# Optimization experiments

Hardware: AMD Instinct MI355X
Metric: run time of the kernel (lower is better)

Reference implementation:

```python
import jax, jax.numpy as jnp
import numpy as np

SEQ_LEN, BATCH, D_IN, D_H, D_OUT = 512, 64, 1024, 1024, 1024
W_SCALE = 0.02  # small init so sigmoid/tanh stay in a sane range


def setup_inputs() -> dict:
    key = jax.random.key(0)
    ks = jax.random.split(key, 12)
    rn = lambda k, shape: jax.random.normal(k, shape, dtype=jnp.float32)
    return {
        "x_seq": rn(ks[0], (SEQ_LEN, BATCH, D_IN)),
        "h0": jnp.zeros((BATCH, D_H), dtype=jnp.float32),
        "Wxz_w": rn(ks[1], (D_H, D_IN)) * W_SCALE,
        "Wxz_b": rn(ks[2], (D_H,)) * W_SCALE,
        "Whz_w": rn(ks[3], (D_H, D_H)) * W_SCALE,
        "Wxr_w": rn(ks[4], (D_H, D_IN)) * W_SCALE,
        "Wxr_b": rn(ks[5], (D_H,)) * W_SCALE,
        "Whr_w": rn(ks[6], (D_H, D_H)) * W_SCALE,
        "Wxn_w": rn(ks[7], (D_H, D_IN)) * W_SCALE,
        "Wxn_b": rn(ks[8], (D_H,)) * W_SCALE,
        "Whn_w": rn(ks[9], (D_H, D_H)) * W_SCALE,
        "Why_w": rn(ks[10], (D_OUT, D_H)) * W_SCALE,
        "Why_b": rn(ks[11], (D_OUT,)) * W_SCALE,
    }


def reference(x_seq, h0, Wxz_w, Wxz_b, Whz_w, Wxr_w, Wxr_b, Whr_w,
              Wxn_w, Wxn_b, Whn_w, Why_w, Why_b):
    # Precompute all input projections in one batched GEMM per gate:
    # (S, B, D_in) @ (D_in, D_h) -> (S, B, D_h). torch Linear: x @ W.T + b.
    xz = jnp.einsum('sbi,hi->sbh', x_seq, Wxz_w) + Wxz_b
    xr = jnp.einsum('sbi,hi->sbh', x_seq, Wxr_w) + Wxr_b
    xn = jnp.einsum('sbi,hi->sbh', x_seq, Wxn_w) + Wxn_b

    def step(h, xs):
        xz_t, xr_t, xn_t = xs
        z = jax.nn.sigmoid(xz_t + h @ Whz_w.T)
        r = jax.nn.sigmoid(xr_t + h @ Whr_w.T)
        n = jnp.tanh(xn_t + (r * h) @ Whn_w.T)
        h_new = (1.0 - z) * h + z * n
        return h_new, h_new

    h_last, hs = jax.lax.scan(step, h0, (xz, xr, xn))  # hs: (S, B, D_h)
    outputs = jnp.einsum('sbh,oh->sbo', hs, Why_w) + Why_b
    return outputs, h_last
```

## Files before the change

### kernel.cpp

```cpp
#include <hip/hip_runtime.h>

typedef unsigned int uint;
typedef unsigned short ushort;
typedef unsigned long long u64;

typedef short s8v __attribute__((ext_vector_type(8)));
typedef float f4v __attribute__((ext_vector_type(4)));

#define S_LEN 512
#define BATCH 64
#define DH    1024
#define DIN   1024

union B8 { s8v v; uint u[4]; u64 ull[2]; ushort s[8]; };

__device__ inline ushort f2bf(float f){
  uint u = __builtin_bit_cast(uint, f);
  u += 0x7fffu + ((u >> 16) & 1u);
  return (ushort)(u >> 16);
}
__device__ inline float bf2f(ushort s){
  uint u = ((uint)s) << 16;
  return __builtin_bit_cast(float, u);
}

__device__ inline f4v mfma16(s8v a, s8v b, f4v c){
  return __builtin_amdgcn_mfma_f32_16x16x32_bf16(a, b, c, 0, 0, 0);
}

__device__ inline s8v ld_b8(const ushort* p){
  return *reinterpret_cast<const s8v*>(p);
}

__device__ inline s8v ld_b8_llc(const ushort* p){
  B8 b;
  const u64* q = (const u64*)p;
  b.ull[0] = __hip_atomic_load(q,   __ATOMIC_RELAXED, __HIP_MEMORY_SCOPE_AGENT);
  b.ull[1] = __hip_atomic_load(q+1, __ATOMIC_RELAXED, __HIP_MEMORY_SCOPE_AGENT);
  return b.v;
}

__device__ inline uint ald32(const uint* p){
  return __hip_atomic_load(p, __ATOMIC_RELAXED, __HIP_MEMORY_SCOPE_AGENT);
}
__device__ inline void ast32(uint* p, uint v){
  __hip_atomic_store(p, v, __ATOMIC_RELAXED, __HIP_MEMORY_SCOPE_AGENT);
}

__device__ inline s8v cvt8(float4 a, float4 b){
  B8 r;
  r.s[0]=f2bf(a.x); r.s[1]=f2bf(a.y); r.s[2]=f2bf(a.z); r.s[3]=f2bf(a.w);
  r.s[4]=f2bf(b.x); r.s[5]=f2bf(b.y); r.s[6]=f2bf(b.z); r.s[7]=f2bf(b.w);
  return r.v;
}

__global__ void cvt_kernel(const float* __restrict__ src, ushort* __restrict__ dst, int n){
  int i = (blockIdx.x * blockDim.x + threadIdx.x) * 4;
  if (i + 3 < n){
    float4 v = *reinterpret_cast<const float4*>(src + i);
    u64 p = (u64)f2bf(v.x)
          | ((u64)f2bf(v.y) << 16)
          | ((u64)f2bf(v.z) << 32)
          | ((u64)f2bf(v.w) << 48);
    *reinterpret_cast<u64*>(dst + i) = p;
  }
}

__global__ void __launch_bounds__(256, 1)
proj3_kernel(const float* __restrict__ X,
             const ushort* __restrict__ W0, const ushort* __restrict__ W1, const ushort* __restrict__ W2,
             const float* __restrict__ bias0, const float* __restrict__ bias1, const float* __restrict__ bias2,
             ushort* __restrict__ C0, ushort* __restrict__ C1, ushort* __restrict__ C2)
{
  const int lane = threadIdx.x & 63;
  const int wave = threadIdx.x >> 6;
  const int l15  = lane & 15;
  const int krow = (lane >> 4) << 3;
  const int n0 = blockIdx.x * 64;
  const int m0 = blockIdx.y * 128 + wave * 32;

  const ushort* Ws[3] = {W0, W1, W2};
  const float*  Bs[3] = {bias0, bias1, bias2};
  ushort*       Cs[3] = {C0, C1, C2};

  f4v acc[2][3][4];
  #pragma unroll
  for (int ms = 0; ms < 2; ++ms)
    #pragma unroll
    for (int g = 0; g < 3; ++g)
      #pragma unroll
      for (int nn = 0; nn < 4; ++nn)
        acc[ms][g][nn] = (f4v){0.f,0.f,0.f,0.f};

  const float* a0 = X + (m0 + l15) * DIN + krow;
  const float* a1 = a0 + 16 * DIN;

  for (int k = 0; k < DIN; k += 32){
    s8v af[2];
    {
      const float4* p0 = reinterpret_cast<const float4*>(a0 + k);
      const float4* p1 = reinterpret_cast<const float4*>(a1 + k);
      af[0] = cvt8(p0[0], p0[1]);
      af[1] = cvt8(p1[0], p1[1]);
    }
    #pragma unroll
    for (int g = 0; g < 3; ++g){
      const ushort* W = Ws[g];
      #pragma unroll
      for (int nn = 0; nn < 4; ++nn){
        s8v bfr = ld_b8(W + (n0 + nn*16 + l15) * DIN + k + krow);
        acc[0][g][nn] = mfma16(af[0], bfr, acc[0][g][nn]);
        acc[1][g][nn] = mfma16(af[1], bfr, acc[1][g][nn]);
      }
    }
  }

  #pragma unroll
  for (int g = 0; g < 3; ++g){
    ushort* C = Cs[g];
    #pragma unroll
    for (int nn = 0; nn < 4; ++nn){
      const int n = n0 + nn*16 + l15;
      const float bv = Bs[g][n];
      #pragma unroll
      for (int ms = 0; ms < 2; ++ms){
        #pragma unroll
        for (int r = 0; r < 4; ++r){
          int m = m0 + ms*16 + ((lane>>4)<<2) + r;
          C[m * DH + n] = f2bf(acc[ms][g][nn][r] + bv);
        }
      }
    }
  }
}

__global__ void __launch_bounds__(256, 1)
gemm1_kernel(const ushort* __restrict__ A, const ushort* __restrict__ W,
             const float* __restrict__ bias, float* __restrict__ C)
{
  const int lane = threadIdx.x & 63;
  const int wave = threadIdx.x >> 6;
  const int l15  = lane & 15;
  const int krow = (lane >> 4) << 3;
  const int n0 = blockIdx.x * 128;
  const int m0 = blockIdx.y * 128 + wave * 32;

  f4v acc[2][8];
  #pragma unroll
  for (int ms = 0; ms < 2; ++ms)
    #pragma unroll
    for (int nn = 0; nn < 8; ++nn)
      acc[ms][nn] = (f4v){0.f,0.f,0.f,0.f};

  const ushort* a0 = A + (m0 + l15) * DH + krow;
  const ushort* a1 = a0 + 16 * DH;

  for (int k = 0; k < DH; k += 32){
    s8v af0 = ld_b8(a0 + k);
    s8v af1 = ld_b8(a1 + k);
    #pragma unroll
    for (int nn = 0; nn < 8; ++nn){
      s8v b = ld_b8(W + (n0 + nn*16 + l15) * DH + k + krow);
      acc[0][nn] = mfma16(af0, b, acc[0][nn]);
      acc[1][nn] = mfma16(af1, b, acc[1][nn]);
    }
  }

  #pragma unroll
  for (int nn = 0; nn < 8; ++nn){
    const int n = n0 + nn*16 + l15;
    const float bv = bias[n];
    #pragma unroll
    for (int ms = 0; ms < 2; ++ms){
      #pragma unroll
      for (int r = 0; r < 4; ++r){
        int m = m0 + ms*16 + ((lane>>4)<<2) + r;
        C[m * DH + n] = acc[ms][nn][r] + bv;
      }
    }
  }
}

__global__ void __launch_bounds__(256, 1)
scan_kernel(const ushort* __restrict__ xz, const ushort* __restrict__ xr,
            const ushort* __restrict__ xn,
            const ushort* __restrict__ Whz, const ushort* __restrict__ Whr,
            const ushort* __restrict__ Whn,
            const float* __restrict__ h0,
            ushort* __restrict__ hbuf,
            ushort* __restrict__ rhbuf,
            ushort* __restrict__ hs,
            float*  __restrict__ hlast,
            uint* __restrict__ hflags,
            uint* __restrict__ rhflags)
{
  const int tid  = threadIdx.x;
  const int wave = tid >> 6;
  const int lane = tid & 63;
  const int l15  = lane & 15;
  const int hi2  = lane >> 4;
  const int krow = hi2 << 3;
  const int wid  = blockIdx.x;
  const int g    = wid >> 5;
  const int jt   = wid & 31;
  const int b0   = g << 4;
  const int j0   = jt << 5;
  const int kbase = wave << 8;

  __shared__ float redA[2][4][512];
  __shared__ float redB[4][512];

  s8v wz[2][8], wr[2][8], wn[2][8];
  #pragma unroll
  for (int nn = 0; nn < 2; ++nn){
    const int wbase = (j0 + nn*16 + l15) * DH + kbase + krow;
    #pragma unroll
    for (int kk = 0; kk < 8; ++kk){
      wz[nn][kk] = ld_b8(Whz + wbase + kk*32);
      wr[nn][kk] = ld_b8(Whr + wbase + kk*32);
      wn[nn][kk] = ld_b8(Whn + wbase + kk*32);
    }
  }

  const int bl   = tid >> 4;
  const int jl2  = (tid & 15) << 1;
  const int brow = b0 + bl;
  const int jcol = j0 + jl2;
  float2 h2 = *reinterpret_cast<const float2*>(h0 + brow * DH + jcol);
  float hr0 = h2.x, hr1 = h2.y;

  const int arow = b0 + l15;
  const uint* hfp  = hflags  + (g*32 + wave*8 + (l15 & 7)) * 4;
  const uint* rhfp = rhflags + (g*32 + wave*8 + (l15 & 7)) * 4;
  uint* rhdst = (uint*)(rhbuf) ;
  (void)rhdst;

  {
    uint pack = (uint)f2bf(hr0) | ((uint)f2bf(hr1) << 16);
    ast32((uint*)(hbuf + 64*1024 + brow*DH + jcol), pack);
  }
  __syncthreads();
  if (tid == 0)
    ast32(&hflags[wid*4], 1u);

  float z0 = 0.f, z1 = 0.f;

  #pragma unroll 1
  for (int t = 0; t < S_LEN; ++t){
    const int xidx = (t * BATCH + brow) * DH + jcol;

    uint xzp = *reinterpret_cast<const uint*>(xz + xidx);
    uint xrp = *reinterpret_cast<const uint*>(xr + xidx);
    float xzv0 = bf2f((ushort)(xzp & 0xFFFFu)), xzv1 = bf2f((ushort)(xzp >> 16));
    float xrv0 = bf2f((ushort)(xrp & 0xFFFFu)), xrv1 = bf2f((ushort)(xrp >> 16));

    {
      const uint tgt = (uint)(t + 1);
      while (true){
        uint v = ald32(hfp);
        if (__all(v >= tgt)) break;
        __builtin_amdgcn_s_sleep(2);
      }
    }
    __asm__ volatile("" ::: "memory");

    f4v az[2] = {(f4v){0.f,0.f,0.f,0.f}, (f4v){0.f,0.f,0.f,0.f}};
    f4v ar[2] = {(f4v){0.f,0.f,0.f,0.f}, (f4v){0.f,0.f,0.f,0.f}};
    {
      const ushort* ap = hbuf + ((t ^ 1) & 1) * (64*1024) + arow * DH + kbase + krow;
      #pragma unroll
      for (int kk = 0; kk < 8; ++kk){
        s8v a = ld_b8_llc(ap + kk*32);
        az[0] = mfma16(a, wz[0][kk], az[0]);
        az[1] = mfma16(a, wz[1][kk], az[1]);
        ar[0] = mfma16(a, wr[0][kk], ar[0]);
        ar[1] = mfma16(a, wr[1][kk], ar[1]);
      }
    }
    #pragma unroll
    for (int nn = 0; nn < 2; ++nn)
      #pragma unroll
      for (int r = 0; r < 4; ++r){
        const int e = (hi2*4 + r)*32 + nn*16 + l15;
        redA[0][wave][e] = az[nn][r];
        redA[1][wave][e] = ar[nn][r];
      }
    __syncthreads();

    const int e0 = bl*32 + jl2;
    float sz0 = redA[0][0][e0]   + redA[0][1][e0]   + redA[0][2][e0]   + redA[0][3][e0];
    float sz1 = redA[0][0][e0+1] + redA[0][1][e0+1] + redA[0][2][e0+1] + redA[0][3][e0+1];
    float sr0 = redA[1][0][e0]   + redA[1][1][e0]   + redA[1][2][e0]   + redA[1][3][e0];
    float sr1 = redA[1][0][e0+1] + redA[1][1][e0+1] + redA[1][2][e0+1] + redA[1][3][e0+1];
    z0 = 1.f / (1.f + __expf(-(xzv0 + sz0)));
    z1 = 1.f / (1.f + __expf(-(xzv1 + sz1)));
    float r0 = 1.f / (1.f + __expf(-(xrv0 + sr0)));
    float r1 = 1.f / (1.f + __expf(-(xrv1 + sr1)));
    float rh0 = r0 * hr0;
    float rh1 = r1 * hr1;
    {
      uint pack = (uint)f2bf(rh0) | ((uint)f2bf(rh1) << 16);
      ast32((uint*)(rhbuf + (t & 1)*(64*1024) + brow*DH + jcol), pack);
    }
    __syncthreads();
    if (tid == 0)
      ast32(&rhflags[wid*4], (uint)(t + 1));

    uint xnp = *reinterpret_cast<const uint*>(xn + xidx);
    float xnv0 = bf2f((ushort)(xnp & 0xFFFFu)), xnv1 = bf2f((ushort)(xnp >> 16));

    {
      const uint tgt = (uint)(t + 1);
      while (true){
        uint v = ald32(rhfp);
        if (__all(v >= tgt)) break;
        __builtin_amdgcn_s_sleep(2);
      }
    }
    __asm__ volatile("" ::: "memory");

    f4v an[2] = {(f4v){0.f,0.f,0.f,0.f}, (f4v){0.f,0.f,0.f,0.f}};
    {
      const ushort* ap = rhbuf + (t & 1)*(64*1024) + arow * DH + kbase + krow;
      #pragma unroll
      for (int kk = 0; kk < 8; ++kk){
        s8v a = ld_b8_llc(ap + kk*32);
        an[0] = mfma16(a, wn[0][kk], an[0]);
        an[1] = mfma16(a, wn[1][kk], an[1]);
      }
    }
    #pragma unroll
    for (int nn = 0; nn < 2; ++nn)
      #pragma unroll
      for (int r = 0; r < 4; ++r){
        const int e = (hi2*4 + r)*32 + nn*16 + l15;
        redB[wave][e] = an[nn][r];
      }
    __syncthreads();

    float sn0 = redB[0][e0]   + redB[1][e0]   + redB[2][e0]   + redB[3][e0];
    float sn1 = redB[0][e0+1] + redB[1][e0+1] + redB[2][e0+1] + redB[3][e0+1];
    float pre0 = xnv0 + sn0;
    float pre1 = xnv1 + sn1;
    float e_0 = __expf(2.f * pre0);
    float e_1 = __expf(2.f * pre1);
    float n0 = 1.f - 2.f / (e_0 + 1.f);
    float n1 = 1.f - 2.f / (e_1 + 1.f);
    float hn0 = hr0 + z0 * (n0 - hr0);
    float hn1 = hr1 + z1 * (n1 - hr1);
    hr0 = hn0; hr1 = hn1;

    {
      uint pack = (uint)f2bf(hn0) | ((uint)f2bf(hn1) << 16);
      ast32((uint*)(hbuf + (t & 1)*(64*1024) + brow*DH + jcol), pack);
      *reinterpret_cast<uint*>(hs + xidx) = pack;
      if (t == S_LEN - 1){
        float2 hl; hl.x = hn0; hl.y = hn1;
        *reinterpret_cast<float2*>(hlast + brow*DH + jcol) = hl;
      }
    }
    __syncthreads();
    if (tid == 0)
      ast32(&hflags[wid*4], (uint)(t + 2));
  }
}

extern "C" void kernel_launch(void* const* d_in, const int* in_sizes, int n_in,
                              void* d_out, int out_size, void* d_ws, size_t ws_size,
                              hipStream_t stream) {
  const float* x_seq = (const float*)d_in[0];
  const float* h0    = (const float*)d_in[1];
  const float* Wxz_w = (const float*)d_in[2];
  const float* Wxz_b = (const float*)d_in[3];
  const float* Whz_w = (const float*)d_in[4];
  const float* Wxr_w = (const float*)d_in[5];
  const float* Wxr_b = (const float*)d_in[6];
  const float* Whr_w = (const float*)d_in[7];
  const float* Wxn_w = (const float*)d_in[8];
  const float* Wxn_b = (const float*)d_in[9];
  const float* Whn_w = (const float*)d_in[10];
  const float* Why_w = (const float*)d_in[11];
  const float* Why_b = (const float*)d_in[12];

  const size_t MiB = 1u << 20;
  unsigned char* ws = (unsigned char*)d_ws;

  ushort* Whz16 = (ushort*)(ws + 0*MiB);
  ushort* Whr16 = (ushort*)(ws + 2*MiB);
  ushort* Whn16 = (ushort*)(ws + 4*MiB);
  ushort* Wxz16 = (ushort*)(ws + 6*MiB);
  ushort* Wxr16 = (ushort*)(ws + 8*MiB);
  ushort* Wxn16 = (ushort*)(ws + 10*MiB);
  ushort* Why16 = (ushort*)(ws + 12*MiB);
  ushort* xn_buf = (ushort*)(ws + 16*MiB);
  ushort* hs     = (ushort*)(ws + 80*MiB);
  ushort* hbuf   = (ushort*)(ws + 144*MiB);
  ushort* rhbuf  = (ushort*)(ws + 144*MiB + 256*1024);
  uint*   hflags = (uint*)  (ws + 144*MiB + 512*1024);
  uint*   rhflags= (uint*)  (ws + 144*MiB + 512*1024 + 2048);

  ushort* xz_buf = (ushort*)d_out;
  ushort* xr_buf = xz_buf + (size_t)S_LEN*BATCH*DH;
  float*  out_f  = (float*)d_out;
  float*  hlast  = out_f + (size_t)S_LEN*BATCH*DH;

  const int NW = DH * DIN;

  cvt_kernel<<<1024, 256, 0, stream>>>(Whz_w, Whz16, NW);
  cvt_kernel<<<1024, 256, 0, stream>>>(Whr_w, Whr16, NW);
  cvt_kernel<<<1024, 256, 0, stream>>>(Whn_w, Whn16, NW);
  cvt_kernel<<<1024, 256, 0, stream>>>(Wxz_w, Wxz16, NW);
  cvt_kernel<<<1024, 256, 0, stream>>>(Wxr_w, Wxr16, NW);
  cvt_kernel<<<1024, 256, 0, stream>>>(Wxn_w, Wxn16, NW);
  cvt_kernel<<<1024, 256, 0, stream>>>(Why_w, Why16, NW);

  proj3_kernel<<<dim3(16, 256), 256, 0, stream>>>(
      x_seq, Wxz16, Wxr16, Wxn16, Wxz_b, Wxr_b, Wxn_b, xz_buf, xr_buf, xn_buf);

  hipMemsetAsync((void*)hflags, 0, 4096, stream);

  scan_kernel<<<128, 256, 0, stream>>>(
      xz_buf, xr_buf, xn_buf, Whz16, Whr16, Whn16, h0,
      hbuf, rhbuf, hs, hlast, hflags, rhflags);

  gemm1_kernel<<<dim3(8, 256), 256, 0, stream>>>(hs, Why16, Why_b, out_f);
}
```

Measured before the change: 5.563 ms.

## Split recurrent scan into single-wave blocks with full-K per wave and LDS Whn

The scan kernel moves from 128 blocks of 4 waves, each wave covering a K-quarter and reducing through shared memory, to 256 single-wave blocks that each own 16 output columns and loop over the full K dimension. Whz and Whr stay in registers while Whn is placed in LDS, and h/rh loads are double-buffered in groups of eight. This removes the LDS reductions and __syncthreads per step and spreads the work over more CUs. In exchange each wave issues more serial MFMAs per step, and twice as many flags must be polled per barrier.

```diff
diff --git a/kernel.cpp b/kernel.cpp
--- a/kernel.cpp
+++ b/kernel.cpp
@@ -11,6 +11,7 @@
 #define BATCH 64
 #define DH    1024
 #define DIN   1024
+#define HSZ   (64*1024)
 
 union B8 { s8v v; uint u[4]; u64 ull[2]; ushort s[8]; };
 
@@ -53,6 +54,17 @@
   r.s[4]=f2bf(b.x); r.s[5]=f2bf(b.y); r.s[6]=f2bf(b.z); r.s[7]=f2bf(b.w);
   return r.v;
 }
+
+#define LOAD8(B, base, q) do { \
+  B[0] = ld_b8_llc((base) + (q)*256 +   0); \
+  B[1] = ld_b8_llc((base) + (q)*256 +  32); \
+  B[2] = ld_b8_llc((base) + (q)*256 +  64); \
+  B[3] = ld_b8_llc((base) + (q)*256 +  96); \
+  B[4] = ld_b8_llc((base) + (q)*256 + 128); \
+  B[5] = ld_b8_llc((base) + (q)*256 + 160); \
+  B[6] = ld_b8_llc((base) + (q)*256 + 192); \
+  B[7] = ld_b8_llc((base) + (q)*256 + 224); \
+} while(0)
 
 __global__ void cvt_kernel(const float* __restrict__ src, ushort* __restrict__ dst, int n){
   int i = (blockIdx.x * blockDim.x + threadIdx.x) * 4;
@@ -181,7 +193,7 @@
   }
 }
 
-__global__ void __launch_bounds__(256, 1)
+__global__ void __launch_bounds__(64, 1)
 scan_kernel(const ushort* __restrict__ xz, const ushort* __restrict__ xr,
             const ushort* __restrict__ xn,
             const ushort* __restrict__ Whz, const ushort* __restrict__ Whr,
@@ -194,174 +206,175 @@
             uint* __restrict__ hflags,
             uint* __restrict__ rhflags)
 {
-  const int tid  = threadIdx.x;
-  const int wave = tid >> 6;
-  const int lane = tid & 63;
+  const int lane = threadIdx.x;
   const int l15  = lane & 15;
   const int hi2  = lane >> 4;
-  const int krow = hi2 << 3;
   const int wid  = blockIdx.x;
-  const int g    = wid >> 5;
-  const int jt   = wid & 31;
+  const int g    = wid >> 6;
+  const int jt   = wid & 63;
   const int b0   = g << 4;
-  const int j0   = jt << 5;
-  const int kbase = wave << 8;
-
-  __shared__ float redA[2][4][512];
-  __shared__ float redB[4][512];
-
-  s8v wz[2][8], wr[2][8], wn[2][8];
-  #pragma unroll
-  for (int nn = 0; nn < 2; ++nn){
-    const int wbase = (j0 + nn*16 + l15) * DH + kbase + krow;
-    #pragma unroll
-    for (int kk = 0; kk < 8; ++kk){
-      wz[nn][kk] = ld_b8(Whz + wbase + kk*32);
-      wr[nn][kk] = ld_b8(Whr + wbase + kk*32);
-      wn[nn][kk] = ld_b8(Whn + wbase + kk*32);
-    }
-  }
-
-  const int bl   = tid >> 4;
-  const int jl2  = (tid & 15) << 1;
-  const int brow = b0 + bl;
-  const int jcol = j0 + jl2;
-  float2 h2 = *reinterpret_cast<const float2*>(h0 + brow * DH + jcol);
-  float hr0 = h2.x, hr1 = h2.y;
-
-  const int arow = b0 + l15;
-  const uint* hfp  = hflags  + (g*32 + wave*8 + (l15 & 7)) * 4;
-  const uint* rhfp = rhflags + (g*32 + wave*8 + (l15 & 7)) * 4;
-  uint* rhdst = (uint*)(rhbuf) ;
-  (void)rhdst;
-
+  const int j0   = jt << 4;
+
+  __shared__ s8v wn_lds[32][64];
+
+  s8v wz[32], wr[32];
   {
-    uint pack = (uint)f2bf(hr0) | ((uint)f2bf(hr1) << 16);
-    ast32((uint*)(hbuf + 64*1024 + brow*DH + jcol), pack);
-  }
-  __syncthreads();
-  if (tid == 0)
-    ast32(&hflags[wid*4], 1u);
-
-  float z0 = 0.f, z1 = 0.f;
+    const int wcol = (j0 + l15) * DH + hi2 * 8;
+    #pragma unroll
+    for (int f = 0; f < 32; ++f){
+      wz[f] = ld_b8(Whz + wcol + f*32);
+      wr[f] = ld_b8(Whr + wcol + f*32);
+      wn_lds[f][lane] = ld_b8(Whn + wcol + f*32);
+    }
+  }
+
+  float hreg[4];
+  #pragma unroll
+  for (int r = 0; r < 4; ++r)
+    hreg[r] = h0[(b0 + hi2*4 + r)*DH + j0 + l15];
+
+  #pragma unroll
+  for (int r = 0; r < 4; ++r){
+    ushort mybf = f2bf(hreg[r]);
+    uint other = (uint)(ushort)__shfl_xor((int)mybf, 1, 64);
+    if ((lane & 1) == 0){
+      uint pack = (uint)mybf | (other << 16);
+      ast32((uint*)(hbuf + HSZ + (b0 + hi2*4 + r)*DH + j0 + l15), pack);
+    }
+  }
+  __asm__ volatile("s_waitcnt vmcnt(0)" ::: "memory");
+  if (lane == 0) ast32(&hflags[wid*4], 1u);
+
+  const uint* hfp  = hflags  + (g*64 + lane) * 4;
+  const uint* rhfp = rhflags + (g*64 + lane) * 4;
+
+  s8v A0[8], A1[8];
 
   #pragma unroll 1
   for (int t = 0; t < S_LEN; ++t){
-    const int xidx = (t * BATCH + brow) * DH + jcol;
-
-    uint xzp = *reinterpret_cast<const uint*>(xz + xidx);
-    uint xrp = *reinterpret_cast<const uint*>(xr + xidx);
-    float xzv0 = bf2f((ushort)(xzp & 0xFFFFu)), xzv1 = bf2f((ushort)(xzp >> 16));
-    float xrv0 = bf2f((ushort)(xrp & 0xFFFFu)), xrv1 = bf2f((ushort)(xrp >> 16));
+    const size_t xb = (size_t)(t*BATCH + b0 + hi2*4) * DH + j0 + l15;
+    float xzv[4], xrv[4], xnv[4];
+    #pragma unroll
+    for (int r = 0; r < 4; ++r){
+      xzv[r] = bf2f(xz[xb + (size_t)r*DH]);
+      xrv[r] = bf2f(xr[xb + (size_t)r*DH]);
+      xnv[r] = bf2f(xn[xb + (size_t)r*DH]);
+    }
 
     {
       const uint tgt = (uint)(t + 1);
       while (true){
         uint v = ald32(hfp);
         if (__all(v >= tgt)) break;
-        __builtin_amdgcn_s_sleep(2);
+        __builtin_amdgcn_s_sleep(1);
       }
     }
     __asm__ volatile("" ::: "memory");
 
+    const ushort* ap = hbuf + ((t ^ 1) & 1) * HSZ + (b0 + l15) * DH + hi2*8;
+    LOAD8(A0, ap, 0);
+    LOAD8(A1, ap, 1);
     f4v az[2] = {(f4v){0.f,0.f,0.f,0.f}, (f4v){0.f,0.f,0.f,0.f}};
     f4v ar[2] = {(f4v){0.f,0.f,0.f,0.f}, (f4v){0.f,0.f,0.f,0.f}};
-    {
-      const ushort* ap = hbuf + ((t ^ 1) & 1) * (64*1024) + arow * DH + kbase + krow;
-      #pragma unroll
-      for (int kk = 0; kk < 8; ++kk){
-        s8v a = ld_b8_llc(ap + kk*32);
-        az[0] = mfma16(a, wz[0][kk], az[0]);
-        az[1] = mfma16(a, wz[1][kk], az[1]);
-        ar[0] = mfma16(a, wr[0][kk], ar[0]);
-        ar[1] = mfma16(a, wr[1][kk], ar[1]);
-      }
-    }
-    #pragma unroll
-    for (int nn = 0; nn < 2; ++nn)
-      #pragma unroll
-      for (int r = 0; r < 4; ++r){
-        const int e = (hi2*4 + r)*32 + nn*16 + l15;
-        redA[0][wave][e] = az[nn][r];
-        redA[1][wave][e] = ar[nn][r];
-      }
-    __syncthreads();
-
-    const int e0 = bl*32 + jl2;
-    float sz0 = redA[0][0][e0]   + redA[0][1][e0]   + redA[0][2][e0]   + redA[0][3][e0];
-    float sz1 = redA[0][0][e0+1] + redA[0][1][e0+1] + redA[0][2][e0+1] + redA[0][3][e0+1];
-    float sr0 = redA[1][0][e0]   + redA[1][1][e0]   + redA[1][2][e0]   + redA[1][3][e0];
-    float sr1 = redA[1][0][e0+1] + redA[1][1][e0+1] + redA[1][2][e0+1] + redA[1][3][e0+1];
-    z0 = 1.f / (1.f + __expf(-(xzv0 + sz0)));
-    z1 = 1.f / (1.f + __expf(-(xzv1 + sz1)));
-    float r0 = 1.f / (1.f + __expf(-(xrv0 + sr0)));
-    float r1 = 1.f / (1.f + __expf(-(xrv1 + sr1)));
-    float rh0 = r0 * hr0;
-    float rh1 = r1 * hr1;
-    {
-      uint pack = (uint)f2bf(rh0) | ((uint)f2bf(rh1) << 16);
-      ast32((uint*)(rhbuf + (t & 1)*(64*1024) + brow*DH + jcol), pack);
-    }
-    __syncthreads();
-    if (tid == 0)
-      ast32(&rhflags[wid*4], (uint)(t + 1));
-
-    uint xnp = *reinterpret_cast<const uint*>(xn + xidx);
-    float xnv0 = bf2f((ushort)(xnp & 0xFFFFu)), xnv1 = bf2f((ushort)(xnp >> 16));
+    #pragma unroll
+    for (int i = 0; i < 8; ++i){
+      az[i&1] = mfma16(A0[i], wz[i], az[i&1]);
+      ar[i&1] = mfma16(A0[i], wr[i], ar[i&1]);
+    }
+    LOAD8(A0, ap, 2);
+    #pragma unroll
+    for (int i = 0; i < 8; ++i){
+      az[i&1] = mfma16(A1[i], wz[8+i], az[i&1]);
+      ar[i&1] = mfma16(A1[i], wr[8+i], ar[i&1]);
+    }
+    LOAD8(A1, ap, 3);
+    #pragma unroll
+    for (int i = 0; i < 8; ++i){
+      az[i&1] = mfma16(A0[i], wz[16+i], az[i&1]);
+      ar[i&1] = mfma16(A0[i], wr[16+i], ar[i&1]);
+    }
+    #pragma unroll
+    for (int i = 0; i < 8; ++i){
+      az[i&1] = mfma16(A1[i], wz[24+i], az[i&1]);
+      ar[i&1] = mfma16(A1[i], wr[24+i], ar[i&1]);
+    }
+
+    float zz[4], rh[4];
+    #pragma unroll
+    for (int r = 0; r < 4; ++r){
+      float sz = az[0][r] + az[1][r];
+      float sr = ar[0][r] + ar[1][r];
+      zz[r] = 1.f / (1.f + __expf(-(xzv[r] + sz)));
+      float rv = 1.f / (1.f + __expf(-(xrv[r] + sr)));
+      rh[r] = rv * hreg[r];
+    }
+    #pragma unroll
+    for (int r = 0; r < 4; ++r){
+      ushort mybf = f2bf(rh[r]);
+      uint other = (uint)(ushort)__shfl_xor((int)mybf, 1, 64);
+      if ((lane & 1) == 0){
+        uint pack = (uint)mybf | (other << 16);
+        ast32((uint*)(rhbuf + (t & 1)*HSZ + (b0 + hi2*4 + r)*DH + j0 + l15), pack);
+      }
+    }
+    __asm__ volatile("s_waitcnt vmcnt(0)" ::: "memory");
+    if (lane == 0) ast32(&rhflags[wid*4], (uint)(t + 1));
 
     {
       const uint tgt = (uint)(t + 1);
       while (true){
         uint v = ald32(rhfp);
         if (__all(v >= tgt)) break;
-        __builtin_amdgcn_s_sleep(2);
+        __builtin_amdgcn_s_sleep(1);
       }
     }
     __asm__ volatile("" ::: "memory");
 
+    const ushort* rp = rhbuf + (t & 1) * HSZ + (b0 + l15) * DH + hi2*8;
+    LOAD8(A0, rp, 0);
+    LOAD8(A1, rp, 1);
     f4v an[2] = {(f4v){0.f,0.f,0.f,0.f}, (f4v){0.f,0.f,0.f,0.f}};
-    {
-      const ushort* ap = rhbuf + (t & 1)*(64*1024) + arow * DH + kbase + krow;
+    #pragma unroll
+    for (int i = 0; i < 8; ++i)
+      an[i&1] = mfma16(A0[i], wn_lds[i][lane], an[i&1]);
+    LOAD8(A0, rp, 2);
+    #pragma unroll
+    for (int i = 0; i < 8; ++i)
+      an[i&1] = mfma16(A1[i], wn_lds[8+i][lane], an[i&1]);
+    LOAD8(A1, rp, 3);
+    #pragma unroll
+    for (int i = 0; i < 8; ++i)
+      an[i&1] = mfma16(A0[i], wn_lds[16+i][lane], an[i&1]);
+    #pragma unroll
+    for (int i = 0; i < 8; ++i)
+      an[i&1] = mfma16(A1[i], wn_lds[24+i][lane], an[i&1]);
+
+    #pragma unroll
+    for (int r = 0; r < 4; ++r){
+      float pre = xnv[r] + an[0][r] + an[1][r];
+      float e = __expf(2.f * pre);
+      float nv = 1.f - 2.f / (e + 1.f);
+      hreg[r] = hreg[r] + zz[r] * (nv - hreg[r]);
+    }
+
+    #pragma unroll
+    for (int r = 0; r < 4; ++r){
+      ushort mybf = f2bf(hreg[r]);
+      uint other = (uint)(ushort)__shfl_xor((int)mybf, 1, 64);
+      const int row = b0 + hi2*4 + r;
+      if ((lane & 1) == 0){
+        uint pack = (uint)mybf | (other << 16);
+        ast32((uint*)(hbuf + (t & 1)*HSZ + row*DH + j0 + l15), pack);
+        *reinterpret_cast<uint*>(hs + (size_t)(t*BATCH + row)*DH + j0 + l15) = pack;
+      }
+    }
+    if (t == S_LEN - 1){
       #pragma unroll
-      for (int kk = 0; kk < 8; ++kk){
-        s8v a = ld_b8_llc(ap + kk*32);
-        an[0] = mfma16(a, wn[0][kk], an[0]);
-        an[1] = mfma16(a, wn[1][kk], an[1]);
-      }
-    }
-    #pragma unroll
-    for (int nn = 0; nn < 2; ++nn)
-      #pragma unroll
-      for (int r = 0; r < 4; ++r){
-        const int e = (hi2*4 + r)*32 + nn*16 + l15;
-        redB[wave][e] = an[nn][r];
-      }
-    __syncthreads();
-
-    float sn0 = redB[0][e0]   + redB[1][e0]   + redB[2][e0]   + redB[3][e0];
-    float sn1 = redB[0][e0+1] + redB[1][e0+1] + redB[2][e0+1] + redB[3][e0+1];
-    float pre0 = xnv0 + sn0;
-    float pre1 = xnv1 + sn1;
-    float e_0 = __expf(2.f * pre0);
-    float e_1 = __expf(2.f * pre1);
-    float n0 = 1.f - 2.f / (e_0 + 1.f);
-    float n1 = 1.f - 2.f / (e_1 + 1.f);
-    float hn0 = hr0 + z0 * (n0 - hr0);
-    float hn1 = hr1 + z1 * (n1 - hr1);
-    hr0 = hn0; hr1 = hn1;
-
-    {
-      uint pack = (uint)f2bf(hn0) | ((uint)f2bf(hn1) << 16);
-      ast32((uint*)(hbuf + (t & 1)*(64*1024) + brow*DH + jcol), pack);
-      *reinterpret_cast<uint*>(hs + xidx) = pack;
-      if (t == S_LEN - 1){
-        float2 hl; hl.x = hn0; hl.y = hn1;
-        *reinterpret_cast<float2*>(hlast + brow*DH + jcol) = hl;
-      }
-    }
-    __syncthreads();
-    if (tid == 0)
-      ast32(&hflags[wid*4], (uint)(t + 2));
+      for (int r = 0; r < 4; ++r)
+        hlast[(b0 + hi2*4 + r)*DH + j0 + l15] = hreg[r];
+    }
+    __asm__ volatile("s_waitcnt vmcnt(0)" ::: "memory");
+    if (lane == 0) ast32(&hflags[wid*4], (uint)(t + 2));
   }
 }
 
@@ -397,7 +410,7 @@
   ushort* hbuf   = (ushort*)(ws + 144*MiB);
   ushort* rhbuf  = (ushort*)(ws + 144*MiB + 256*1024);
   uint*   hflags = (uint*)  (ws + 144*MiB + 512*1024);
-  uint*   rhflags= (uint*)  (ws + 144*MiB + 512*1024 + 2048);
+  uint*   rhflags= (uint*)  (ws + 144*MiB + 512*1024 + 4096);
 
   ushort* xz_buf = (ushort*)d_out;
   ushort* xr_buf = xz_buf + (size_t)S_LEN*BATCH*DH;
@@ -417,9 +430,9 @@
   proj3_kernel<<<dim3(16, 256), 256, 0, stream>>>(
       x_seq, Wxz16, Wxr16, Wxn16, Wxz_b, Wxr_b, Wxn_b, xz_buf, xr_buf, xn_buf);
 
-  hipMemsetAsync((void*)hflags, 0, 4096, stream);
-
-  scan_kernel<<<128, 256, 0, stream>>>(
+  hipMemsetAsync((void*)hflags, 0, 8192, stream);
+
+  scan_kernel<<<256, 64, 0, stream>>>(
       xz_buf, xr_buf, xn_buf, Whz16, Whr16, Whn16, h0,
       hbuf, rhbuf, hs, hlast, hflags, rhflags);
 
```

Result: slower. 9.851 ms (+77.1%).

## Replace per-block flag barriers with tag bits embedded in bf16 data

Applied to the files above, without the earlier changes.

Removes the separate hflags/rhflags counters, the __syncthreads before each flag publish, and the double-buffered h/rh arrays. Each packed bf16 pair now carries a step-parity tag in the low mantissa bit of its first element, and consumers poll the data itself until every tag matches, so waiting and loading happen in one pass. This cuts one barrier-plus-flag round trip per phase and lets consumers start as soon as their specific inputs land. In exchange it drops one mantissa bit of h and r*h, and adds a spin guard with an abort flag that silently breaks out after a fixed number of retries, which could produce wrong results under heavy contention.

```diff
diff --git a/kernel.cpp b/kernel.cpp
--- a/kernel.cpp
+++ b/kernel.cpp
@@ -32,14 +32,9 @@
   return *reinterpret_cast<const s8v*>(p);
 }
 
-__device__ inline s8v ld_b8_llc(const ushort* p){
-  B8 b;
-  const u64* q = (const u64*)p;
-  b.ull[0] = __hip_atomic_load(q,   __ATOMIC_RELAXED, __HIP_MEMORY_SCOPE_AGENT);
-  b.ull[1] = __hip_atomic_load(q+1, __ATOMIC_RELAXED, __HIP_MEMORY_SCOPE_AGENT);
-  return b.v;
-}
-
+__device__ inline u64 ald64(const u64* p){
+  return __hip_atomic_load(p, __ATOMIC_RELAXED, __HIP_MEMORY_SCOPE_AGENT);
+}
 __device__ inline uint ald32(const uint* p){
   return __hip_atomic_load(p, __ATOMIC_RELAXED, __HIP_MEMORY_SCOPE_AGENT);
 }
@@ -52,6 +47,44 @@
   r.s[0]=f2bf(a.x); r.s[1]=f2bf(a.y); r.s[2]=f2bf(a.z); r.s[3]=f2bf(a.w);
   r.s[4]=f2bf(b.x); r.s[5]=f2bf(b.y); r.s[6]=f2bf(b.z); r.s[7]=f2bf(b.w);
   return r.v;
+}
+
+#define TAGMASK 0x0000000100000001ull
+__device__ inline u64 tagpat(uint tag){
+  return (u64)(tag & 1u) | ((u64)((tag >> 1) & 1u) << 32);
+}
+
+__device__ inline void poll16(const u64* __restrict__ p, uint tag, B8 (&fr)[8],
+                              uint* __restrict__ abortv){
+  const u64 pat = tagpat(tag);
+  #pragma unroll
+  for (int i = 0; i < 8; ++i){
+    fr[i].ull[0] = ald64(p + i*8);
+    fr[i].ull[1] = ald64(p + i*8 + 1);
+  }
+  uint pend = 0xFFFFu;
+  int guard = 0;
+  while (true){
+    uint np = 0;
+    #pragma unroll
+    for (int i = 0; i < 8; ++i){
+      if ((pend >> (2*i)) & 1u)
+        if (((fr[i].ull[0] ^ pat) & TAGMASK) != 0) np |= 1u << (2*i);
+      if ((pend >> (2*i+1)) & 1u)
+        if (((fr[i].ull[1] ^ pat) & TAGMASK) != 0) np |= 1u << (2*i+1);
+    }
+    pend = np;
+    if (__all(pend == 0)) break;
+    ++guard;
+    if (guard > 8192){ ast32(abortv, 1u); break; }
+    if ((guard & 63) == 0 && ald32(abortv) != 0) break;
+    __builtin_amdgcn_s_sleep(1);
+    #pragma unroll
+    for (int i = 0; i < 8; ++i){
+      if ((pend >> (2*i)) & 1u)   fr[i].ull[0] = ald64(p + i*8);
+      if ((pend >> (2*i+1)) & 1u) fr[i].ull[1] = ald64(p + i*8 + 1);
+    }
+  }
 }
 
 __global__ void cvt_kernel(const float* __restrict__ src, ushort* __restrict__ dst, int n){
@@ -191,8 +224,7 @@
             ushort* __restrict__ rhbuf,
             ushort* __restrict__ hs,
             float*  __restrict__ hlast,
-            uint* __restrict__ hflags,
-            uint* __restrict__ rhflags)
+            uint*   __restrict__ abortv)
 {
   const int tid  = threadIdx.x;
   const int wave = tid >> 6;
@@ -226,23 +258,21 @@
   const int jl2  = (tid & 15) << 1;
   const int brow = b0 + bl;
   const int jcol = j0 + jl2;
+  const uint myb = (uint)((jl2 >> 1) & 1);
   float2 h2 = *reinterpret_cast<const float2*>(h0 + brow * DH + jcol);
   float hr0 = h2.x, hr1 = h2.y;
 
-  const int arow = b0 + l15;
-  const uint* hfp  = hflags  + (g*32 + wave*8 + (l15 & 7)) * 4;
-  const uint* rhfp = rhflags + (g*32 + wave*8 + (l15 & 7)) * 4;
-  uint* rhdst = (uint*)(rhbuf) ;
-  (void)rhdst;
-
   {
-    uint pack = (uint)f2bf(hr0) | ((uint)f2bf(hr1) << 16);
-    ast32((uint*)(hbuf + 64*1024 + brow*DH + jcol), pack);
-  }
-  __syncthreads();
-  if (tid == 0)
-    ast32(&hflags[wid*4], 1u);
-
+    uint tbit = myb ? 0u : 1u;
+    uint pack = ((uint)(f2bf(hr0) & 0xFFFEu) | tbit) | ((uint)f2bf(hr1) << 16);
+    ast32((uint*)(hbuf + brow*DH + jcol), pack);
+  }
+
+  const u64* hpo  = (const u64*)(hbuf  + (b0 + l15)*DH + kbase + krow);
+  const u64* rhpo = (const u64*)(rhbuf + (b0 + l15)*DH + kbase + krow);
+  const int e0 = bl*32 + jl2;
+
+  B8 fr[8];
   float z0 = 0.f, z1 = 0.f;
 
   #pragma unroll 1
@@ -251,31 +281,19 @@
 
     uint xzp = *reinterpret_cast<const uint*>(xz + xidx);
     uint xrp = *reinterpret_cast<const uint*>(xr + xidx);
-    float xzv0 = bf2f((ushort)(xzp & 0xFFFFu)), xzv1 = bf2f((ushort)(xzp >> 16));
-    float xrv0 = bf2f((ushort)(xrp & 0xFFFFu)), xrv1 = bf2f((ushort)(xrp >> 16));
-
-    {
-      const uint tgt = (uint)(t + 1);
-      while (true){
-        uint v = ald32(hfp);
-        if (__all(v >= tgt)) break;
-        __builtin_amdgcn_s_sleep(2);
-      }
-    }
-    __asm__ volatile("" ::: "memory");
+    uint xnp = *reinterpret_cast<const uint*>(xn + xidx);
+
+    poll16(hpo, (uint)(t + 1) & 3u, fr, abortv);
 
     f4v az[2] = {(f4v){0.f,0.f,0.f,0.f}, (f4v){0.f,0.f,0.f,0.f}};
     f4v ar[2] = {(f4v){0.f,0.f,0.f,0.f}, (f4v){0.f,0.f,0.f,0.f}};
-    {
-      const ushort* ap = hbuf + ((t ^ 1) & 1) * (64*1024) + arow * DH + kbase + krow;
-      #pragma unroll
-      for (int kk = 0; kk < 8; ++kk){
-        s8v a = ld_b8_llc(ap + kk*32);
-        az[0] = mfma16(a, wz[0][kk], az[0]);
-        az[1] = mfma16(a, wz[1][kk], az[1]);
-        ar[0] = mfma16(a, wr[0][kk], ar[0]);
-        ar[1] = mfma16(a, wr[1][kk], ar[1]);
-      }
+    #pragma unroll
+    for (int kk = 0; kk < 8; ++kk){
+      s8v a = fr[kk].v;
+      az[0] = mfma16(a, wz[0][kk], az[0]);
+      az[1] = mfma16(a, wz[1][kk], az[1]);
+      ar[0] = mfma16(a, wr[0][kk], ar[0]);
+      ar[1] = mfma16(a, wr[1][kk], ar[1]);
     }
     #pragma unroll
     for (int nn = 0; nn < 2; ++nn)
@@ -287,61 +305,43 @@
       }
     __syncthreads();
 
-    const int e0 = bl*32 + jl2;
     float sz0 = redA[0][0][e0]   + redA[0][1][e0]   + redA[0][2][e0]   + redA[0][3][e0];
     float sz1 = redA[0][0][e0+1] + redA[0][1][e0+1] + redA[0][2][e0+1] + redA[0][3][e0+1];
     float sr0 = redA[1][0][e0]   + redA[1][1][e0]   + redA[1][2][e0]   + redA[1][3][e0];
     float sr1 = redA[1][0][e0+1] + redA[1][1][e0+1] + redA[1][2][e0+1] + redA[1][3][e0+1];
-    z0 = 1.f / (1.f + __expf(-(xzv0 + sz0)));
-    z1 = 1.f / (1.f + __expf(-(xzv1 + sz1)));
-    float r0 = 1.f / (1.f + __expf(-(xrv0 + sr0)));
-    float r1 = 1.f / (1.f + __expf(-(xrv1 + sr1)));
+    z0 = 1.f / (1.f + __expf(-(bf2f((ushort)(xzp & 0xFFFFu)) + sz0)));
+    z1 = 1.f / (1.f + __expf(-(bf2f((ushort)(xzp >> 16))     + sz1)));
+    float r0 = 1.f / (1.f + __expf(-(bf2f((ushort)(xrp & 0xFFFFu)) + sr0)));
+    float r1 = 1.f / (1.f + __expf(-(bf2f((ushort)(xrp >> 16))     + sr1)));
     float rh0 = r0 * hr0;
     float rh1 = r1 * hr1;
     {
-      uint pack = (uint)f2bf(rh0) | ((uint)f2bf(rh1) << 16);
-      ast32((uint*)(rhbuf + (t & 1)*(64*1024) + brow*DH + jcol), pack);
-    }
-    __syncthreads();
-    if (tid == 0)
-      ast32(&rhflags[wid*4], (uint)(t + 1));
-
-    uint xnp = *reinterpret_cast<const uint*>(xn + xidx);
-    float xnv0 = bf2f((ushort)(xnp & 0xFFFFu)), xnv1 = bf2f((ushort)(xnp >> 16));
-
-    {
-      const uint tgt = (uint)(t + 1);
-      while (true){
-        uint v = ald32(rhfp);
-        if (__all(v >= tgt)) break;
-        __builtin_amdgcn_s_sleep(2);
-      }
-    }
-    __asm__ volatile("" ::: "memory");
+      const uint tg = (uint)(t + 1) & 3u;
+      uint tbit = myb ? ((tg >> 1) & 1u) : (tg & 1u);
+      uint pack = ((uint)(f2bf(rh0) & 0xFFFEu) | tbit) | ((uint)f2bf(rh1) << 16);
+      ast32((uint*)(rhbuf + brow*DH + jcol), pack);
+    }
+
+    poll16(rhpo, (uint)(t + 1) & 3u, fr, abortv);
 
     f4v an[2] = {(f4v){0.f,0.f,0.f,0.f}, (f4v){0.f,0.f,0.f,0.f}};
-    {
-      const ushort* ap = rhbuf + (t & 1)*(64*1024) + arow * DH + kbase + krow;
-      #pragma unroll
-      for (int kk = 0; kk < 8; ++kk){
-        s8v a = ld_b8_llc(ap + kk*32);
-        an[0] = mfma16(a, wn[0][kk], an[0]);
-        an[1] = mfma16(a, wn[1][kk], an[1]);
-      }
+    #pragma unroll
+    for (int kk = 0; kk < 8; ++kk){
+      s8v a = fr[kk].v;
+      an[0] = mfma16(a, wn[0][kk], an[0]);
+      an[1] = mfma16(a, wn[1][kk], an[1]);
     }
     #pragma unroll
     for (int nn = 0; nn < 2; ++nn)
       #pragma unroll
-      for (int r = 0; r < 4; ++r){
-        const int e = (hi2*4 + r)*32 + nn*16 + l15;
-        redB[wave][e] = an[nn][r];
-      }
+      for (int r = 0; r < 4; ++r)
+        redB[wave][(hi2*4 + r)*32 + nn*16 + l15] = an[nn][r];
     __syncthreads();
 
     float sn0 = redB[0][e0]   + redB[1][e0]   + redB[2][e0]   + redB[3][e0];
     float sn1 = redB[0][e0+1] + redB[1][e0+1] + redB[2][e0+1] + redB[3][e0+1];
-    float pre0 = xnv0 + sn0;
-    float pre1 = xnv1 + sn1;
+    float pre0 = bf2f((ushort)(xnp & 0xFFFFu)) + sn0;
+    float pre1 = bf2f((ushort)(xnp >> 16))     + sn1;
     float e_0 = __expf(2.f * pre0);
     float e_1 = __expf(2.f * pre1);
     float n0 = 1.f - 2.f / (e_0 + 1.f);
@@ -350,18 +350,18 @@
     float hn1 = hr1 + z1 * (n1 - hr1);
     hr0 = hn0; hr1 = hn1;
 
+    uint cpack = (uint)f2bf(hn0) | ((uint)f2bf(hn1) << 16);
+    *reinterpret_cast<uint*>(hs + xidx) = cpack;
     {
-      uint pack = (uint)f2bf(hn0) | ((uint)f2bf(hn1) << 16);
-      ast32((uint*)(hbuf + (t & 1)*(64*1024) + brow*DH + jcol), pack);
-      *reinterpret_cast<uint*>(hs + xidx) = pack;
-      if (t == S_LEN - 1){
-        float2 hl; hl.x = hn0; hl.y = hn1;
-        *reinterpret_cast<float2*>(hlast + brow*DH + jcol) = hl;
-      }
-    }
-    __syncthreads();
-    if (tid == 0)
-      ast32(&hflags[wid*4], (uint)(t + 2));
+      const uint tg = (uint)(t + 2) & 3u;
+      uint tbit = myb ? ((tg >> 1) & 1u) : (tg & 1u);
+      uint tpack = (cpack & ~1u) | tbit;
+      ast32((uint*)(hbuf + brow*DH + jcol), tpack);
+    }
+    if (t == S_LEN - 1){
+      float2 hl; hl.x = hn0; hl.y = hn1;
+      *reinterpret_cast<float2*>(hlast + brow*DH + jcol) = hl;
+    }
   }
 }
 
@@ -395,9 +395,8 @@
   ushort* xn_buf = (ushort*)(ws + 16*MiB);
   ushort* hs     = (ushort*)(ws + 80*MiB);
   ushort* hbuf   = (ushort*)(ws + 144*MiB);
-  ushort* rhbuf  = (ushort*)(ws + 144*MiB + 256*1024);
-  uint*   hflags = (uint*)  (ws + 144*MiB + 512*1024);
-  uint*   rhflags= (uint*)  (ws + 144*MiB + 512*1024 + 2048);
+  ushort* rhbuf  = (ushort*)(ws + 144*MiB + 128*1024);
+  uint*   abortv = (uint*)  (ws + 144*MiB + 256*1024);
 
   ushort* xz_buf = (ushort*)d_out;
   ushort* xr_buf = xz_buf + (size_t)S_LEN*BATCH*DH;
@@ -417,11 +416,11 @@
   proj3_kernel<<<dim3(16, 256), 256, 0, stream>>>(
       x_seq, Wxz16, Wxr16, Wxn16, Wxz_b, Wxr_b, Wxn_b, xz_buf, xr_buf, xn_buf);
 
-  hipMemsetAsync((void*)hflags, 0, 4096, stream);
+  hipMemsetAsync((void*)hbuf, 0, 256*1024 + 4096, stream);
 
   scan_kernel<<<128, 256, 0, stream>>>(
       xz_buf, xr_buf, xn_buf, Whz16, Whr16, Whn16, h0,
-      hbuf, rhbuf, hs, hlast, hflags, rhflags);
+      hbuf, rhbuf, hs, hlast, abortv);
 
   gemm1_kernel<<<dim3(8, 256), 256, 0, stream>>>(hs, Why16, Why_b, out_f);
 }
```

Result: slower. 7.341 ms (+32.0%).
